# Kernel optimization log

Hardware: AMD Instinct MI355X
Metric: run time of the kernel (lower is better)

## Reference

```python
import jax, jax.numpy as jnp
import numpy as np

B, NS, NT, C = 32, 1000, 100, 256
LAMBDA_GIOU, LAMBDA_L1 = 10.0, 1.0


def _lsa(cost):
    """Hungarian / Jonker-Volgenant shortest-augmenting-path (numpy, O(n^2 m)).
    Matches scipy.optimize.linear_sum_assignment for rectangular matrices."""
    cost = np.asarray(cost, dtype=np.float64)
    transposed = cost.shape[0] > cost.shape[1]
    if transposed:
        cost = cost.T
    n, m = cost.shape  # n <= m
    INF = np.inf
    u = np.zeros(n + 1)
    v = np.zeros(m + 1)
    p = np.zeros(m + 1, dtype=np.int64)   # p[j] = row (1-based) assigned to col j
    way = np.zeros(m + 1, dtype=np.int64)
    for i in range(1, n + 1):
        p[0] = i
        j0 = 0
        minv = np.full(m + 1, INF)
        used = np.zeros(m + 1, dtype=bool)
        while True:
            used[j0] = True
            i0 = p[j0]
            cur = cost[i0 - 1, :] - u[i0] - v[1:]
            free = ~used[1:]
            better = free & (cur < minv[1:])
            minv[1:][better] = cur[better]
            way[1:][better] = j0
            masked = np.where(free, minv[1:], INF)
            j1 = int(np.argmin(masked)) + 1
            delta = masked[j1 - 1]
            u[p[used]] += delta
            v[used] -= delta
            minv[~used] -= delta
            j0 = j1
            if p[j0] == 0:
                break
        while j0:
            j1 = way[j0]
            p[j0] = p[j1]
            j0 = j1
    rows = p[1:] - 1
    cols = np.arange(m)
    keep = rows >= 0
    rows, cols = rows[keep], cols[keep]
    if transposed:
        rows, cols = cols, rows
    order = np.argsort(rows)
    return rows[order], cols[order]


def _pairwise_cost(logits, classes, sb, tb):
    """Per-batch (Ns,Nt) cost = CE(logits_s, class_t) + 10*(1-GIoU(box_s, box_t)) + L1mean."""
    Bc, Ns, Cd = logits.shape
    Nt = classes.shape[1]
    # Cross entropy: logsumexp over classes minus logit at target class (identical
    # math to the torch expand+flatten CE, without the Ns*Nt*C copy).
    lse = jax.nn.logsumexp(logits, axis=-1)  # (B,Ns)
    picked = jnp.take_along_axis(
        logits, jnp.broadcast_to(classes[:, None, :], (Bc, Ns, Nt)), axis=2)  # (B,Ns,Nt)
    ce = lse[:, :, None] - picked
    # Pairwise GIoU (boxes in xyxy)
    s = sb[:, :, None, :]  # (B,Ns,1,4)
    t = tb[:, None, :, :]  # (B,1,Nt,4)
    ix1 = jnp.maximum(s[..., 0], t[..., 0])
    iy1 = jnp.maximum(s[..., 1], t[..., 1])
    ix2 = jnp.minimum(s[..., 2], t[..., 2])
    iy2 = jnp.minimum(s[..., 3], t[..., 3])
    inter = jnp.clip(ix2 - ix1, 0.0) * jnp.clip(iy2 - iy1, 0.0)
    area_s = (s[..., 2] - s[..., 0]) * (s[..., 3] - s[..., 1])
    area_t = (t[..., 2] - t[..., 0]) * (t[..., 3] - t[..., 1])
    union = area_s + area_t - inter
    iou = inter / union
    cx1 = jnp.minimum(s[..., 0], t[..., 0])
    cy1 = jnp.minimum(s[..., 1], t[..., 1])
    cx2 = jnp.maximum(s[..., 2], t[..., 2])
    cy2 = jnp.maximum(s[..., 3], t[..., 3])
    carea = (cx2 - cx1) * (cy2 - cy1)
    giou = iou - (carea - union) / carea
    l1 = jnp.abs(s - t).mean(axis=-1)  # (B,Ns,Nt)
    return ce + LAMBDA_GIOU * (1.0 - giou) + LAMBDA_L1 * l1


def _valid_boxes(key, b, n):
    p = jax.random.uniform(key, (b, n, 2, 2), dtype=jnp.float32)
    lo = p.min(axis=2)
    hi = p.max(axis=2)
    return jnp.concatenate([lo, hi], axis=-1)  # (b,n,4) xyxy, x1<x2, y1<y2


def setup_inputs() -> dict:
    key = jax.random.key(0)
    k1, k2, k3, k4 = jax.random.split(key, 4)
    return {
        "source_class_logits": jax.random.normal(k1, (B, NS, C), dtype=jnp.float32),
        "target_classes": jax.random.randint(k2, (B, NT), 0, C, dtype=jnp.int32),
        "source_boxes": _valid_boxes(k3, B, NS),
        "target_boxes": _valid_boxes(k4, B, NT),
    }


def reference(source_class_logits, target_classes, source_boxes, target_boxes):
    cost = _pairwise_cost(source_class_logits, target_classes, source_boxes, target_boxes)
    cost_np = np.asarray(cost)
    rows_l, cols_l = [], []
    for b in range(cost_np.shape[0]):  # assignment is inherently per-matrix / host-side
        r, c = _lsa(cost_np[b])
        rows_l.append(r)
        cols_l.append(c)
    rows = jnp.asarray(np.stack(rows_l))  # (B, min(Ns,Nt))
    cols = jnp.asarray(np.stack(cols_l))
    bidx = jnp.arange(cost.shape[0])[:, None]
    return cost[bidx, rows, cols].mean(axis=1)  # (B,)
```

## Files before the change

### kernel.cpp

```cpp
#include <hip/hip_runtime.h>
#include <math.h>

#define NSRC 1000
#define NTGT 100
#define NCLS 256
#define NB   32
#define NSP  1024
#define PAD_IDX(j) ((j) + ((j) >> 4))
#define LDSN (NSP + (NSP >> 4))
#define AUCTION_EPS 0.04f
#define NWAVES 8
#define ROUND_CAP 96


__global__ __launch_bounds__(256) void lse_kernel(const float* __restrict__ logits,
                                                  float* __restrict__ lse) {
    int wid  = threadIdx.x >> 6;
    int lane = threadIdx.x & 63;
    int row0 = blockIdx.x * 32 + wid * 8;
    #pragma unroll 2
    for (int r = 0; r < 8; ++r) {
        int row = row0 + r;
        float4 v4 = reinterpret_cast<const float4*>(logits + (size_t)row * NCLS)[lane];
        float m = fmaxf(fmaxf(v4.x, v4.y), fmaxf(v4.z, v4.w));
        #pragma unroll
        for (int off = 32; off >= 1; off >>= 1) m = fmaxf(m, __shfl_xor(m, off));
        float s = expf(v4.x - m) + expf(v4.y - m) + expf(v4.z - m) + expf(v4.w - m);
        #pragma unroll
        for (int off = 32; off >= 1; off >>= 1) s += __shfl_xor(s, off);
        if (lane == 0) lse[row] = m + logf(s);
    }
}

__global__ __launch_bounds__(256) void cost_kernel(const float* __restrict__ logits,
                                                   const int*   __restrict__ tcls,
                                                   const float* __restrict__ sbox,
                                                   const float* __restrict__ tbox,
                                                   const float* __restrict__ lse,
                                                   float*       __restrict__ cost,
                                                   float*       __restrict__ urow_g,
                                                   int*         __restrict__ jmin_g,
                                                   float*       __restrict__ m2_g) {
    int b  = blockIdx.x & 31;
    int t  = blockIdx.x >> 5;
    int bt = b * NTGT + t;
    int cls = tcls[bt];
    float4 tb = reinterpret_cast<const float4*>(tbox)[bt];
    float area_t = (tb.z - tb.x) * (tb.w - tb.y);
    float* crow = cost + (size_t)bt * NSP;
    float m1 = 1e38f, m2 = 1e38f; int mi = 0x7fffffff;
    for (int s = threadIdx.x; s < NSP; s += 256) {
        if (s >= NSRC) { crow[s] = 1e30f; continue; }
        int gs = b * NSRC + s;
        float4 sb = reinterpret_cast<const float4*>(sbox)[gs];
        float ce = lse[gs] - logits[(size_t)gs * NCLS + cls];
        float ix1 = fmaxf(sb.x, tb.x), iy1 = fmaxf(sb.y, tb.y);
        float ix2 = fminf(sb.z, tb.z), iy2 = fminf(sb.w, tb.w);
        float inter = fmaxf(ix2 - ix1, 0.f) * fmaxf(iy2 - iy1, 0.f);
        float area_s = (sb.z - sb.x) * (sb.w - sb.y);
        float uni = area_s + area_t - inter;
        float iou = inter / uni;
        float cx1 = fminf(sb.x, tb.x), cy1 = fminf(sb.y, tb.y);
        float cx2 = fmaxf(sb.z, tb.z), cy2 = fmaxf(sb.w, tb.w);
        float carea = (cx2 - cx1) * (cy2 - cy1);
        float giou = iou - (carea - uni) / carea;
        float l1 = 0.25f * (fabsf(sb.x - tb.x) + fabsf(sb.y - tb.y) +
                            fabsf(sb.z - tb.z) + fabsf(sb.w - tb.w));
        float c = ce + 10.0f * (1.0f - giou) + l1;
        crow[s] = c;
        if (c < m1) { m2 = m1; m1 = c; mi = s; }
        else if (c < m2) m2 = c;
    }
    #pragma unroll
    for (int off = 32; off >= 1; off >>= 1) {
        float om1 = __shfl_xor(m1, off);
        float om2 = __shfl_xor(m2, off);
        int   oi  = __shfl_xor(mi, off);
        bool take = (om1 < m1) || (om1 == m1 && oi < mi);
        float lose = take ? m1 : om1;
        m1 = take ? om1 : m1;
        mi = take ? oi  : mi;
        m2 = fminf(fminf(m2, om2), lose);
    }
    __shared__ float smin[4], smin2[4];
    __shared__ int   sidx[4];
    int wid = threadIdx.x >> 6, lane = threadIdx.x & 63;
    if (lane == 0) { smin[wid] = m1; smin2[wid] = m2; sidx[wid] = mi; }
    __syncthreads();
    if (threadIdx.x == 0) {
        #pragma unroll
        for (int w = 1; w < 4; ++w) {
            float om1 = smin[w], om2 = smin2[w]; int oi = sidx[w];
            bool take = (om1 < m1) || (om1 == m1 && oi < mi);
            float lose = take ? m1 : om1;
            m1 = take ? om1 : m1;
            mi = take ? oi  : mi;
            m2 = fminf(fminf(m2, om2), lose);
        }
        urow_g[bt] = m1;
        jmin_g[bt] = mi;
        m2_g[bt]   = m2;
    }
}

__global__ __launch_bounds__(512) void lsa_kernel(const float* __restrict__ cost,
                                                  const float* __restrict__ urow_g,
                                                  const int*   __restrict__ jmin_g,
                                                  const float* __restrict__ m2_g,
                                                  float* __restrict__ out) {
    int b    = blockIdx.x;
    int tid  = threadIdx.x;
    int wv   = tid >> 6;
    int lane = tid & 63;
    const float* C = cost + (size_t)b * NTGT * NSP;
    __shared__ int   way[LDSN];
    __shared__ int   pcol[LDSN];
    __shared__ float uu[LDSN];
    __shared__ float vsh[LDSN];
    __shared__ float urow[NTGT];
    __shared__ int   done[NTGT];
    __shared__ float bm1[NTGT];
    __shared__ float bm2[NTGT];
    __shared__ int   bj [NTGT];
    __shared__ float bv [NTGT];
    __shared__ int   qbuf[1024];
    __shared__ int   qstate[2];
    __shared__ int   srow[NWAVES];

    for (int t = tid; t < LDSN; t += 512) {
        pcol[t] = -1; uu[t] = 0.f; vsh[t] = 0.f; way[t] = 0x7fffffff;
    }
    for (int t = tid; t < NTGT; t += 512) {
        float m1 = urow_g[b * NTGT + t];
        urow[t] = m1;
        bm1[t]  = m1;
        bm2[t]  = m2_g[b * NTGT + t];
        bj[t]   = jmin_g[b * NTGT + t];
        bv[t]   = 0.f;
    }
    if (tid == 0) { qstate[0] = 0; qstate[1] = 0; }
    __syncthreads();

    for (int r = tid; r < NTGT; r += 512) atomicMin(&way[PAD_IDX(bj[r])], r);
    __syncthreads();
    for (int r = tid; r < NTGT; r += 512) {
        int j = bj[r];
        int w = (way[PAD_IDX(j)] == r) ? 1 : 0;
        done[r] = w;
        if (w) { pcol[PAD_IDX(j)] = r; uu[PAD_IDX(j)] = urow[r]; }
    }
    __syncthreads();

    if (tid < 64) {
        int qt = 0;
        #pragma unroll
        for (int r0 = 0; r0 < 128; r0 += 64) {
            int r = r0 + lane;
            bool act = (r < NTGT) && !done[r];
            unsigned long long mask = __ballot(act);
            if (act) qbuf[qt + __popcll(mask & ((1ull << lane) - 1ull))] = r;
            qt += __popcll(mask);
        }
        if (lane == 0) qstate[1] = qt;
    }
    __syncthreads();

    int base = lane * 16;

    for (int round = 0; round < ROUND_CAP; ++round) {
        int qh = qstate[0], qt = qstate[1];
        int navail = qt - qh;
        if (navail <= 0) break;
        int take = navail < NWAVES ? navail : NWAVES;
        if (wv < take) {
            int i = qbuf[(qh + wv) & 1023];
            if (lane == 0) srow[wv] = i;
            float m1p = bm1[i] + (bv[i] - vsh[PAD_IDX(bj[i])]);
            if (m1p > bm2[i]) {
                const float4* row4 = reinterpret_cast<const float4*>(C + (size_t)i * NSP + base);
                float m1 = 1e38f, m2 = 1e38f; int j1 = 0x7fffffff;
                #pragma unroll
                for (int q = 0; q < 4; ++q) {
                    float4 c4 = row4[q];
                    float vals[4];
                    vals[0] = c4.x - vsh[PAD_IDX(base + 4*q + 0)];
                    vals[1] = c4.y - vsh[PAD_IDX(base + 4*q + 1)];
                    vals[2] = c4.z - vsh[PAD_IDX(base + 4*q + 2)];
                    vals[3] = c4.w - vsh[PAD_IDX(base + 4*q + 3)];
                    #pragma unroll
                    for (int e = 0; e < 4; ++e) {
                        float val = vals[e];
                        if (val < m1) { m2 = m1; m1 = val; j1 = base + 4*q + e; }
                        else m2 = fminf(m2, val);
                    }
                }
                #pragma unroll
                for (int off = 32; off >= 1; off >>= 1) {
                    float om1 = __shfl_xor(m1, off);
                    float om2 = __shfl_xor(m2, off);
                    int   oj1 = __shfl_xor(j1, off);
                    bool tk = (om1 < m1) || (om1 == m1 && oj1 < j1);
                    float lose = tk ? m1 : om1;
                    m1 = tk ? om1 : m1;
                    j1 = tk ? oj1 : j1;
                    m2 = fminf(fminf(m2, om2), lose);
                }
                if (lane == 0) {
                    bm1[i] = m1; bm2[i] = m2; bj[i] = j1;
                    bv[i]  = vsh[PAD_IDX(j1)];
                }
            }
        }
        __syncthreads();
        if (tid == 0) {
            int qt2 = qstate[1];
            for (int s = 0; s < take; ++s) {
                int i  = srow[s];
                int j1 = bj[i];
                int pj1 = PAD_IDX(j1);
                float vnow = vsh[pj1];
                float m1p  = bm1[i] + (bv[i] - vnow);
                if (m1p <= bm2[i]) {
                    float delta = fmaxf(bm2[i] - m1p, AUCTION_EPS);
                    int old = pcol[pj1];
                    vsh[pj1]  = vnow - delta;
                    pcol[pj1] = i;
                    uu[pj1]   = m1p + delta;
                    urow[i]   = m1p + delta;
                    done[i]   = 1;
                    if (old >= 0) { qbuf[qt2 & 1023] = old; ++qt2; done[old] = 0; }
                } else {
                    qbuf[qt2 & 1023] = i; ++qt2;
                }
            }
            qstate[0] = qstate[0] + take;
            qstate[1] = qt2;
        }
        __syncthreads();
    }

    float v[16], d[16];
    if (tid < 64) {
        #pragma unroll
        for (int k = 0; k < 16; ++k) v[k] = vsh[PAD_IDX(base + k)];
    }
    __syncthreads();

    for (int i = 0; i < NTGT; ++i) {
        if (done[i]) continue;
        float ui = urow[i];
        float Df = 0.f;
        int jf = -1;
        if (tid < 64) {
            const float4* row4 = reinterpret_cast<const float4*>(C + (size_t)i * NSP + base);
            #pragma unroll
            for (int q = 0; q < 4; ++q) {
                float4 c4 = row4[q];
                d[4*q+0] = c4.x - ui - v[4*q+0];
                d[4*q+1] = c4.y - ui - v[4*q+1];
                d[4*q+2] = c4.z - ui - v[4*q+2];
                d[4*q+3] = c4.w - ui - v[4*q+3];
            }
            #pragma unroll
            for (int k = 0; k < 16; ++k) way[PAD_IDX(base + k)] = -1;
            unsigned int used = 0;
            int   pf_j = -1;
            float pfr[16];

            for (int it = 0; it < NTGT + 3; ++it) {
                float l1 = 1e38f, l2 = 1e38f;
                int   i1 = 0x7fffffff, i2 = 0x7fffffff;
                #pragma unroll
                for (int k = 0; k < 16; ++k) {
                    float val = ((used >> k) & 1u) ? 1e38f : d[k];
                    int idx = base + k;
                    if (val < l1) { l2 = l1; i2 = i1; l1 = val; i1 = idx; }
                    else if (val < l2) { l2 = val; i2 = idx; }
                }
                #pragma unroll
                for (int off = 32; off >= 1; off >>= 1) {
                    float ob1 = __shfl_xor(l1, off), ob2 = __shfl_xor(l2, off);
                    int   oc1 = __shfl_xor(i1, off), oc2 = __shfl_xor(i2, off);
                    bool tk = (ob1 < l1) || (ob1 == l1 && oc1 < i1);
                    float n1 = tk ? ob1 : l1; int ni1 = tk ? oc1 : i1;
                    float lz = tk ? l1  : ob1; int liz = tk ? i1  : oc1;
                    float n2 = lz; int ni2 = liz;
                    if (l2  < n2) { n2 = l2;  ni2 = i2;  }
                    if (ob2 < n2) { n2 = ob2; ni2 = oc2; }
                    l1 = n1; i1 = ni1; l2 = n2; i2 = ni2;
                }
                float wmin = l1; int j0 = i1; int j0b = i2;
                if (wmin >= 1e37f) break;
                int pj0 = pcol[PAD_IDX(j0)];
                if (pj0 < 0) { Df = wmin; jf = j0; break; }
                if ((j0 >> 4) == lane) used |= 1u << (j0 & 15);
                float uref = uu[PAD_IDX(j0)];
                float sft  = wmin - uref;
                float cr[16];
                if (pf_j == j0) {
                    #pragma unroll
                    for (int k = 0; k < 16; ++k) cr[k] = pfr[k];
                    pf_j = -1;
                } else {
                    const float4* rr = reinterpret_cast<const float4*>(C + (size_t)pj0 * NSP + base);
                    #pragma unroll
                    for (int q = 0; q < 4; ++q) {
                        float4 c4 = rr[q];
                        cr[4*q+0] = c4.x; cr[4*q+1] = c4.y; cr[4*q+2] = c4.z; cr[4*q+3] = c4.w;
                    }
                }
                if (j0b < NSP && j0b != pf_j) {
                    int pj0b = pcol[PAD_IDX(j0b)];
                    if (pj0b >= 0) {
                        const float4* rb = reinterpret_cast<const float4*>(C + (size_t)pj0b * NSP + base);
                        #pragma unroll
                        for (int q = 0; q < 4; ++q) {
                            float4 c4 = rb[q];
                            pfr[4*q+0] = c4.x; pfr[4*q+1] = c4.y;
                            pfr[4*q+2] = c4.z; pfr[4*q+3] = c4.w;
                        }
                        pf_j = j0b;
                    } else pf_j = -1;
                }
                #pragma unroll
                for (int k = 0; k < 16; ++k) {
                    float cand = sft + cr[k] - v[k];
                    bool upd = (cand < d[k]) && !((used >> k) & 1u);
                    if (upd) { d[k] = cand; way[PAD_IDX(base + k)] = j0; }
                }
            }

            if (jf >= 0) {
                #pragma unroll
                for (int k = 0; k < 16; ++k) {
                    if ((used >> k) & 1u) {
                        float diff = Df - d[k];
                        v[k] -= diff;
                        uu[PAD_IDX(base + k)] += diff;
                    }
                }
            }
        }
        __syncthreads();
        if (tid == 0 && jf >= 0) {
            int j = jf;
            for (int g = 0; g < NSP; ++g) {
                int jp = way[PAD_IDX(j)];
                if (jp < 0) { pcol[PAD_IDX(j)] = i; uu[PAD_IDX(j)] = ui + Df; break; }
                pcol[PAD_IDX(j)] = pcol[PAD_IDX(jp)];
                uu[PAD_IDX(j)]   = uu[PAD_IDX(jp)];
                j = jp;
            }
            done[i] = 1;
        }
        __syncthreads();
    }

    if (tid < 64) {
        float acc = 0.f;
        #pragma unroll
        for (int k = 0; k < 16; ++k) {
            int j = base + k;
            if (j < NSRC) {
                int r = pcol[PAD_IDX(j)];
                if (r >= 0) acc += C[(size_t)r * NSP + j];
            }
        }
        #pragma unroll
        for (int off = 32; off >= 1; off >>= 1) acc += __shfl_xor(acc, off);
        if (lane == 0) out[b] = acc * (1.0f / NTGT);
    }
}

extern "C" void kernel_launch(void* const* d_in, const int* in_sizes, int n_in,
                              void* d_out, int out_size, void* d_ws, size_t ws_size,
                              hipStream_t stream) {
    const float* logits = (const float*)d_in[0];
    const int*   tcls   = (const int*)  d_in[1];
    const float* sbox   = (const float*)d_in[2];
    const float* tbox   = (const float*)d_in[3];
    float* out = (float*)d_out;

    float* lse    = (float*)d_ws;
    float* cost   = lse + 32768;
    float* urow_g = cost + (size_t)NB * NTGT * NSP;
    int*   jmin_g = (int*)(urow_g + NB * NTGT);
    float* m2_g   = (float*)(jmin_g + NB * NTGT);

    lse_kernel <<<1000,      256, 0, stream>>>(logits, lse);
    cost_kernel<<<NB * NTGT, 256, 0, stream>>>(logits, tcls, sbox, tbox, lse, cost,
                                               urow_g, jmin_g, m2_g);
    lsa_kernel <<<NB,        512, 0, stream>>>(cost, urow_g, jmin_g, m2_g, out);
}
```

Baseline: 126.5 us.

## Fuse logsumexp into cost kernel with source-chunk tiling and partial row minima

Removes the separate logsumexp kernel. The cost kernel now tiles over 64-source chunks per batch: each wave computes the LSE per source row and gathers the target-class logits through shuffles into LDS, then computes the GIoU/L1 cost for all targets. Per-chunk min/second-min/argmin partials go to global memory and are merged in the LSA kernel's init. This drops one launch and the scattered per-target logit gathers, but launches only 512 blocks and adds a 16-way merge in the serial LSA kernel.

```diff
diff --git a/kernel.cpp b/kernel.cpp
--- a/kernel.cpp
+++ b/kernel.cpp
@@ -6,6 +6,9 @@
 #define NCLS 256
 #define NB   32
 #define NSP  1024
+#define CHUNK 64
+#define NCHK  16
+#define CEP   101
 #define PAD_IDX(j) ((j) + ((j) >> 4))
 #define LDSN (NSP + (NSP >> 4))
 #define AUCTION_EPS 0.04f
@@ -13,100 +16,109 @@
 #define ROUND_CAP 96
 
 
-__global__ __launch_bounds__(256) void lse_kernel(const float* __restrict__ logits,
-                                                  float* __restrict__ lse) {
-    int wid  = threadIdx.x >> 6;
-    int lane = threadIdx.x & 63;
-    int row0 = blockIdx.x * 32 + wid * 8;
-    #pragma unroll 2
-    for (int r = 0; r < 8; ++r) {
-        int row = row0 + r;
-        float4 v4 = reinterpret_cast<const float4*>(logits + (size_t)row * NCLS)[lane];
-        float m = fmaxf(fmaxf(v4.x, v4.y), fmaxf(v4.z, v4.w));
-        #pragma unroll
-        for (int off = 32; off >= 1; off >>= 1) m = fmaxf(m, __shfl_xor(m, off));
-        float s = expf(v4.x - m) + expf(v4.y - m) + expf(v4.z - m) + expf(v4.w - m);
-        #pragma unroll
-        for (int off = 32; off >= 1; off >>= 1) s += __shfl_xor(s, off);
-        if (lane == 0) lse[row] = m + logf(s);
-    }
-}
-
 __global__ __launch_bounds__(256) void cost_kernel(const float* __restrict__ logits,
                                                    const int*   __restrict__ tcls,
                                                    const float* __restrict__ sbox,
                                                    const float* __restrict__ tbox,
-                                                   const float* __restrict__ lse,
                                                    float*       __restrict__ cost,
-                                                   float*       __restrict__ urow_g,
-                                                   int*         __restrict__ jmin_g,
-                                                   float*       __restrict__ m2_g) {
-    int b  = blockIdx.x & 31;
-    int t  = blockIdx.x >> 5;
-    int bt = b * NTGT + t;
-    int cls = tcls[bt];
-    float4 tb = reinterpret_cast<const float4*>(tbox)[bt];
-    float area_t = (tb.z - tb.x) * (tb.w - tb.y);
-    float* crow = cost + (size_t)bt * NSP;
-    float m1 = 1e38f, m2 = 1e38f; int mi = 0x7fffffff;
-    for (int s = threadIdx.x; s < NSP; s += 256) {
-        if (s >= NSRC) { crow[s] = 1e30f; continue; }
-        int gs = b * NSRC + s;
-        float4 sb = reinterpret_cast<const float4*>(sbox)[gs];
-        float ce = lse[gs] - logits[(size_t)gs * NCLS + cls];
-        float ix1 = fmaxf(sb.x, tb.x), iy1 = fmaxf(sb.y, tb.y);
-        float ix2 = fminf(sb.z, tb.z), iy2 = fminf(sb.w, tb.w);
-        float inter = fmaxf(ix2 - ix1, 0.f) * fmaxf(iy2 - iy1, 0.f);
-        float area_s = (sb.z - sb.x) * (sb.w - sb.y);
-        float uni = area_s + area_t - inter;
-        float iou = inter / uni;
-        float cx1 = fminf(sb.x, tb.x), cy1 = fminf(sb.y, tb.y);
-        float cx2 = fmaxf(sb.z, tb.z), cy2 = fmaxf(sb.w, tb.w);
-        float carea = (cx2 - cx1) * (cy2 - cy1);
-        float giou = iou - (carea - uni) / carea;
-        float l1 = 0.25f * (fabsf(sb.x - tb.x) + fabsf(sb.y - tb.y) +
-                            fabsf(sb.z - tb.z) + fabsf(sb.w - tb.w));
-        float c = ce + 10.0f * (1.0f - giou) + l1;
-        crow[s] = c;
-        if (c < m1) { m2 = m1; m1 = c; mi = s; }
-        else if (c < m2) m2 = c;
-    }
-    #pragma unroll
-    for (int off = 32; off >= 1; off >>= 1) {
-        float om1 = __shfl_xor(m1, off);
-        float om2 = __shfl_xor(m2, off);
-        int   oi  = __shfl_xor(mi, off);
-        bool take = (om1 < m1) || (om1 == m1 && oi < mi);
-        float lose = take ? m1 : om1;
-        m1 = take ? om1 : m1;
-        mi = take ? oi  : mi;
-        m2 = fminf(fminf(m2, om2), lose);
-    }
-    __shared__ float smin[4], smin2[4];
-    __shared__ int   sidx[4];
-    int wid = threadIdx.x >> 6, lane = threadIdx.x & 63;
-    if (lane == 0) { smin[wid] = m1; smin2[wid] = m2; sidx[wid] = mi; }
-    __syncthreads();
-    if (threadIdx.x == 0) {
-        #pragma unroll
-        for (int w = 1; w < 4; ++w) {
-            float om1 = smin[w], om2 = smin2[w]; int oi = sidx[w];
+                                                   float*       __restrict__ pm1,
+                                                   float*       __restrict__ pm2,
+                                                   int*         __restrict__ pmi) {
+    int b     = blockIdx.x & 31;
+    int chunk = blockIdx.x >> 5;
+    int s0    = chunk * CHUNK;
+    int wid   = threadIdx.x >> 6;
+    int lane  = threadIdx.x & 63;
+
+    __shared__ float  ce_lds[CHUNK][CEP];
+    __shared__ float4 sb_lds[CHUNK];
+    __shared__ float4 tb_lds[NTGT];
+    __shared__ int    cls_lds[128];
+
+    for (int t = threadIdx.x; t < NTGT; t += 256) {
+        tb_lds[t]  = reinterpret_cast<const float4*>(tbox)[b * NTGT + t];
+        cls_lds[t] = tcls[b * NTGT + t];
+    }
+    if (threadIdx.x < 128 - NTGT) cls_lds[NTGT + threadIdx.x] = 0;
+    int valid = NSRC - s0; valid = valid > CHUNK ? CHUNK : valid;
+    for (int r = threadIdx.x; r < valid; r += 256)
+        sb_lds[r] = reinterpret_cast<const float4*>(sbox)[b * NSRC + s0 + r];
+    __syncthreads();
+
+    #pragma unroll 2
+    for (int r = wid; r < valid; r += 4) {
+        int gs = b * NSRC + s0 + r;
+        float4 v4 = reinterpret_cast<const float4*>(logits + (size_t)gs * NCLS)[lane];
+        float m = fmaxf(fmaxf(v4.x, v4.y), fmaxf(v4.z, v4.w));
+        #pragma unroll
+        for (int off = 32; off >= 1; off >>= 1) m = fmaxf(m, __shfl_xor(m, off));
+        float s = expf(v4.x - m) + expf(v4.y - m) + expf(v4.z - m) + expf(v4.w - m);
+        #pragma unroll
+        for (int off = 32; off >= 1; off >>= 1) s += __shfl_xor(s, off);
+        float lse = m + logf(s);
+        int c0 = cls_lds[lane];
+        int l0 = c0 >> 2, e0 = c0 & 3;
+        float px = __shfl(v4.x, l0), py = __shfl(v4.y, l0),
+              pz = __shfl(v4.z, l0), pw = __shfl(v4.w, l0);
+        float p0 = e0 == 0 ? px : e0 == 1 ? py : e0 == 2 ? pz : pw;
+        ce_lds[r][lane] = lse - p0;
+        int c1 = cls_lds[64 + lane];
+        int l1s = c1 >> 2, e1 = c1 & 3;
+        float qx = __shfl(v4.x, l1s), qy = __shfl(v4.y, l1s),
+              qz = __shfl(v4.z, l1s), qw = __shfl(v4.w, l1s);
+        float p1 = e1 == 0 ? qx : e1 == 1 ? qy : e1 == 2 ? qz : qw;
+        if (lane < NTGT - 64) ce_lds[r][64 + lane] = lse - p1;
+    }
+    __syncthreads();
+
+    bool vs = lane < valid;
+    float4 sb = sb_lds[vs ? lane : 0];
+    float area_s = (sb.z - sb.x) * (sb.w - sb.y);
+    int sg = s0 + lane;
+    for (int t = wid; t < NTGT; t += 4) {
+        float4 tb = tb_lds[t];
+        float area_t = (tb.z - tb.x) * (tb.w - tb.y);
+        float c = 1e30f;
+        if (vs) {
+            float ce = ce_lds[lane][t];
+            float ix1 = fmaxf(sb.x, tb.x), iy1 = fmaxf(sb.y, tb.y);
+            float ix2 = fminf(sb.z, tb.z), iy2 = fminf(sb.w, tb.w);
+            float inter = fmaxf(ix2 - ix1, 0.f) * fmaxf(iy2 - iy1, 0.f);
+            float uni = area_s + area_t - inter;
+            float iou = inter / uni;
+            float cx1 = fminf(sb.x, tb.x), cy1 = fminf(sb.y, tb.y);
+            float cx2 = fmaxf(sb.z, tb.z), cy2 = fmaxf(sb.w, tb.w);
+            float carea = (cx2 - cx1) * (cy2 - cy1);
+            float giou = iou - (carea - uni) / carea;
+            float l1 = 0.25f * (fabsf(sb.x - tb.x) + fabsf(sb.y - tb.y) +
+                                fabsf(sb.z - tb.z) + fabsf(sb.w - tb.w));
+            c = ce + 10.0f * (1.0f - giou) + l1;
+        }
+        cost[(size_t)(b * NTGT + t) * NSP + sg] = c;
+        float m1 = vs ? c : 1e38f, m2 = 1e38f;
+        int   mi = vs ? sg : 0x7fffffff;
+        #pragma unroll
+        for (int off = 32; off >= 1; off >>= 1) {
+            float om1 = __shfl_xor(m1, off);
+            float om2 = __shfl_xor(m2, off);
+            int   oi  = __shfl_xor(mi, off);
             bool take = (om1 < m1) || (om1 == m1 && oi < mi);
             float lose = take ? m1 : om1;
             m1 = take ? om1 : m1;
             mi = take ? oi  : mi;
             m2 = fminf(fminf(m2, om2), lose);
         }
-        urow_g[bt] = m1;
-        jmin_g[bt] = mi;
-        m2_g[bt]   = m2;
+        if (lane == 0) {
+            int idx = (b * NTGT + t) * NCHK + chunk;
+            pm1[idx] = m1; pm2[idx] = m2; pmi[idx] = mi;
+        }
     }
 }
 
 __global__ __launch_bounds__(512) void lsa_kernel(const float* __restrict__ cost,
-                                                  const float* __restrict__ urow_g,
-                                                  const int*   __restrict__ jmin_g,
-                                                  const float* __restrict__ m2_g,
+                                                  const float* __restrict__ pm1,
+                                                  const float* __restrict__ pm2,
+                                                  const int*   __restrict__ pmi,
                                                   float* __restrict__ out) {
     int b    = blockIdx.x;
     int tid  = threadIdx.x;
@@ -131,11 +143,23 @@
         pcol[t] = -1; uu[t] = 0.f; vsh[t] = 0.f; way[t] = 0x7fffffff;
     }
     for (int t = tid; t < NTGT; t += 512) {
-        float m1 = urow_g[b * NTGT + t];
+        int base16 = (b * NTGT + t) * NCHK;
+        float m1 = pm1[base16], m2 = pm2[base16];
+        int   mi = pmi[base16];
+        #pragma unroll
+        for (int k = 1; k < NCHK; ++k) {
+            float om1 = pm1[base16 + k], om2 = pm2[base16 + k];
+            int   oi  = pmi[base16 + k];
+            bool take = (om1 < m1) || (om1 == m1 && oi < mi);
+            float lose = take ? m1 : om1;
+            m1 = take ? om1 : m1;
+            mi = take ? oi  : mi;
+            m2 = fminf(fminf(m2, om2), lose);
+        }
         urow[t] = m1;
         bm1[t]  = m1;
-        bm2[t]  = m2_g[b * NTGT + t];
-        bj[t]   = jmin_g[b * NTGT + t];
+        bm2[t]  = m2;
+        bj[t]   = mi;
         bv[t]   = 0.f;
     }
     if (tid == 0) { qstate[0] = 0; qstate[1] = 0; }
@@ -381,14 +405,12 @@
     const float* tbox   = (const float*)d_in[3];
     float* out = (float*)d_out;
 
-    float* lse    = (float*)d_ws;
-    float* cost   = lse + 32768;
-    float* urow_g = cost + (size_t)NB * NTGT * NSP;
-    int*   jmin_g = (int*)(urow_g + NB * NTGT);
-    float* m2_g   = (float*)(jmin_g + NB * NTGT);
-
-    lse_kernel <<<1000,      256, 0, stream>>>(logits, lse);
-    cost_kernel<<<NB * NTGT, 256, 0, stream>>>(logits, tcls, sbox, tbox, lse, cost,
-                                               urow_g, jmin_g, m2_g);
-    lsa_kernel <<<NB,        512, 0, stream>>>(cost, urow_g, jmin_g, m2_g, out);
+    float* cost = (float*)d_ws;
+    float* pm1  = cost + (size_t)NB * NTGT * NSP;
+    float* pm2  = pm1 + (size_t)NB * NTGT * NCHK;
+    int*   pmi  = (int*)(pm2 + (size_t)NB * NTGT * NCHK);
+
+    cost_kernel<<<NB * NCHK, 256, 0, stream>>>(logits, tcls, sbox, tbox, cost,
+                                               pm1, pm2, pmi);
+    lsa_kernel <<<NB,        512, 0, stream>>>(cost, pm1, pm2, pmi, out);
 }
```

After: 136.3 us. 7.8% more time.
